# Kernel tuning notes

Hardware: AMD Instinct MI355X
Metric: run time of the kernel (lower is better)

The kernel has to match this reference:

```python
import jax, jax.numpy as jnp
import numpy as np
from jax import lax

T, B, D, H, K, A = 256, 512, 128, 50, 5, 4


def setup_inputs() -> dict:
    key = jax.random.key(0)
    ks = jax.random.split(key, 12)
    s = 0.05
    return {
        "x": jax.random.normal(ks[0], (T, B, D), dtype=jnp.float32),
        "W_in": jax.random.normal(ks[1], (H, D), dtype=jnp.float32) * s,
        "b_in": jax.random.normal(ks[2], (H,), dtype=jnp.float32) * s,
        "W_ctx": jax.random.normal(ks[3], (H, 2 * H), dtype=jnp.float32) * s,
        "b_ctx": jax.random.normal(ks[4], (H,), dtype=jnp.float32) * s,
        "W_key": jax.random.normal(ks[5], (K, H), dtype=jnp.float32) * s,
        "b_key": jax.random.normal(ks[6], (K,), dtype=jnp.float32) * s,
        "W_q": jax.random.normal(ks[7], (K, H), dtype=jnp.float32) * s,
        "b_q": jax.random.normal(ks[8], (K,), dtype=jnp.float32) * s,
        "first_context": jax.random.normal(ks[9], (H,), dtype=jnp.float32) * s,
        "W_act": jax.random.normal(ks[10], (A, H), dtype=jnp.float32) * s,
        "b_act": jax.random.normal(ks[11], (A,), dtype=jnp.float32) * s,
    }


def reference(x, W_in, b_in, W_ctx, b_ctx, W_key, b_key, W_q, b_q,
              first_context, W_act, b_act):
    # Unrolls the torch module's per-step forward() over T steps with a
    # growing attention context (horizon=-1 => attend to full history).
    Tn, Bn, _ = x.shape
    Hn = W_in.shape[0]
    Kn = W_key.shape[0]
    neg_inf = jnp.float32(-1e30)

    c0 = jnp.broadcast_to(first_context[None, :], (Bn, Hn))  # [B,H]
    ctx_buf = jnp.zeros((Tn + 1, Bn, Hn), x.dtype).at[0].set(c0)
    key_buf = jnp.zeros((Tn + 1, Bn, Kn), x.dtype).at[0].set(c0 @ W_key.T + b_key)
    step_ids = jnp.arange(Tn + 1)[:, None]  # [T+1,1]

    def step(carry, xt):
        ctx_buf, key_buf, prev_c, t = carry
        h = jax.nn.relu(xt @ W_in.T + b_in)                           # [B,H]
        c = jax.nn.relu(jnp.concatenate([prev_c, h], axis=1) @ W_ctx.T + b_ctx)
        ctx_buf = ctx_buf.at[t + 1].set(c)
        key_buf = key_buf.at[t + 1].set(c @ W_key.T + b_key)
        q = c @ W_q.T + b_q                                           # [B,K]
        scores = jnp.einsum('tbk,bk->tb', key_buf, q)                 # [T+1,B]
        scores = jnp.where(step_ids <= t + 1, scores, neg_inf)
        attn = jax.nn.softmax(scores, axis=0)                         # over history
        w = jnp.einsum('tb,tbh->bh', attn, ctx_buf)                   # [B,H]
        actions = w @ W_act.T + b_act                                 # [B,A]
        return (ctx_buf, key_buf, c, t + 1), actions

    _, actions = lax.scan(step, (ctx_buf, key_buf, c0, jnp.int32(0)), x)
    return actions  # [T,B,A]
```

## Files before the change

kernel.cpp:

```cpp
#include <hip/hip_runtime.h>

#define TT 256
#define BB 512
#define DD 128
#define HH 50
#define KK 5
#define AA 4
#define NROW 131072
#define KQS 260

#define R50(X) X(0) X(1) X(2) X(3) X(4) X(5) X(6) X(7) X(8) X(9) \
  X(10) X(11) X(12) X(13) X(14) X(15) X(16) X(17) X(18) X(19) \
  X(20) X(21) X(22) X(23) X(24) X(25) X(26) X(27) X(28) X(29) \
  X(30) X(31) X(32) X(33) X(34) X(35) X(36) X(37) X(38) X(39) \
  X(40) X(41) X(42) X(43) X(44) X(45) X(46) X(47) X(48) X(49)

typedef _Float16 half4 __attribute__((ext_vector_type(4)));
typedef float f32x4 __attribute__((ext_vector_type(4)));

__global__ void k0_prep(const float* __restrict__ W_in,
                        const float* __restrict__ W_ctx,
                        const float* __restrict__ W_key,
                        const float* __restrict__ W_q,
                        const float* __restrict__ b_key,
                        const float* __restrict__ b_q,
                        float* __restrict__ WHT,
                        float* __restrict__ WK2T, float* __restrict__ bias2) {
  int i = blockIdx.x * 256 + threadIdx.x;
  if (i < HH * 52) {
    int j = i / 52, h = i % 52;
    WHT[i] = (h < HH) ? W_ctx[h * (2 * HH) + HH + j] : 0.f;
  }
  if (i < HH * 64) {
    int j = i >> 6, l = i & 63;
    float v = 0.f;
    if (l < HH) v = W_ctx[l * (2 * HH) + j];
    else if (l < HH + KK) v = W_key[(l - HH) * HH + j];
    else if (l < HH + 2 * KK) v = W_q[(l - HH - KK) * HH + j];
    WK2T[i] = v;
  }
  if (i < 64) {
    float bv = 0.f;
    if (i >= HH && i < HH + KK) bv = b_key[i - HH];
    else if (i >= HH + KK && i < HH + 2 * KK) bv = b_q[i - HH - KK];
    bias2[i] = bv;
  }
}

__global__ __launch_bounds__(256, 2) void k1_mfma(
    const float* __restrict__ x, const float* __restrict__ W_in,
    const float* __restrict__ WHT, const float* __restrict__ b_in,
    const float* __restrict__ b_ctx, _Float16* __restrict__ gh) {
  const int lane = threadIdx.x & 63;
  const int wave = threadIdx.x >> 6;
  const int lrow = lane & 15, lgrp = lane >> 4;

#define WA1D(m, kk)                                                     \
  half4 wa1_##m##_##kk;                                                 \
  {                                                                     \
    const int hh = 16 * (m) + lrow;                                     \
    const int j0 = 16 * (kk) + 4 * lgrp;                                \
    const bool v = (hh < HH);                                           \
    const float* p = W_in + (size_t)(v ? hh : 0) * DD + j0;             \
    wa1_##m##_##kk[0] = (_Float16)(v ? p[0] : 0.f);                     \
    wa1_##m##_##kk[1] = (_Float16)(v ? p[1] : 0.f);                     \
    wa1_##m##_##kk[2] = (_Float16)(v ? p[2] : 0.f);                     \
    wa1_##m##_##kk[3] = (_Float16)(v ? p[3] : 0.f);                     \
  }
  WA1D(0, 0) WA1D(0, 1) WA1D(0, 2) WA1D(0, 3)
  WA1D(0, 4) WA1D(0, 5) WA1D(0, 6) WA1D(0, 7)
  WA1D(1, 0) WA1D(1, 1) WA1D(1, 2) WA1D(1, 3)
  WA1D(1, 4) WA1D(1, 5) WA1D(1, 6) WA1D(1, 7)
  WA1D(2, 0) WA1D(2, 1) WA1D(2, 2) WA1D(2, 3)
  WA1D(2, 4) WA1D(2, 5) WA1D(2, 6) WA1D(2, 7)
  WA1D(3, 0) WA1D(3, 1) WA1D(3, 2) WA1D(3, 3)
  WA1D(3, 4) WA1D(3, 5) WA1D(3, 6) WA1D(3, 7)

#define WA2D(m, kk)                                                     \
  half4 wa2_##m##_##kk;                                                 \
  {                                                                     \
    const int gg = 16 * (m) + lrow;                                     \
    const int h0 = 16 * (kk) + 4 * lgrp;                                \
    wa2_##m##_##kk[0] = (_Float16)((gg < HH && h0 + 0 < HH) ? WHT[(h0 + 0) * 52 + gg] : 0.f); \
    wa2_##m##_##kk[1] = (_Float16)((gg < HH && h0 + 1 < HH) ? WHT[(h0 + 1) * 52 + gg] : 0.f); \
    wa2_##m##_##kk[2] = (_Float16)((gg < HH && h0 + 2 < HH) ? WHT[(h0 + 2) * 52 + gg] : 0.f); \
    wa2_##m##_##kk[3] = (_Float16)((gg < HH && h0 + 3 < HH) ? WHT[(h0 + 3) * 52 + gg] : 0.f); \
  }
  WA2D(0, 0) WA2D(0, 1) WA2D(0, 2) WA2D(0, 3)
  WA2D(1, 0) WA2D(1, 1) WA2D(1, 2) WA2D(1, 3)
  WA2D(2, 0) WA2D(2, 1) WA2D(2, 2) WA2D(2, 3)
  WA2D(3, 0) WA2D(3, 1) WA2D(3, 2) WA2D(3, 3)

#define BDEF(m, r)                                                      \
  const float bin_##m##_##r =                                           \
      (16 * (m) + 4 * lgrp + (r) < HH) ? b_in[16 * (m) + 4 * lgrp + (r)] : 0.f; \
  const float bct_##m##_##r =                                           \
      (16 * (m) + 4 * lgrp + (r) < HH) ? b_ctx[16 * (m) + 4 * lgrp + (r)] : 0.f;
  BDEF(0, 0) BDEF(0, 1) BDEF(0, 2) BDEF(0, 3)
  BDEF(1, 0) BDEF(1, 1) BDEF(1, 2) BDEF(1, 3)
  BDEF(2, 0) BDEF(2, 1) BDEF(2, 2) BDEF(2, 3)
  BDEF(3, 0) BDEF(3, 1) BDEF(3, 2) BDEF(3, 3)

  const f32x4 zf = {0.f, 0.f, 0.f, 0.f};

#pragma unroll 1
  for (int it = 0; it < 4; ++it) {
    const int tile = (blockIdx.x * 4 + wave) * 4 + it;
    const int row = tile * 16 + lrow;
    const float* __restrict__ xr = x + (size_t)row * DD + 4 * lgrp;

#define XLD(kk)                                                         \
  half4 xb##kk;                                                         \
  {                                                                     \
    const float4 xv = *reinterpret_cast<const float4*>(xr + 16 * kk);   \
    xb##kk[0] = (_Float16)xv.x;                                         \
    xb##kk[1] = (_Float16)xv.y;                                         \
    xb##kk[2] = (_Float16)xv.z;                                         \
    xb##kk[3] = (_Float16)xv.w;                                         \
  }
    XLD(0) XLD(1) XLD(2) XLD(3) XLD(4) XLD(5) XLD(6) XLD(7)

    f32x4 d10 = zf, d11 = zf, d12 = zf, d13 = zf;
#define MM1(kk)                                                              \
  d10 = __builtin_amdgcn_mfma_f32_16x16x16f16(wa1_0_##kk, xb##kk, d10, 0, 0, 0); \
  d11 = __builtin_amdgcn_mfma_f32_16x16x16f16(wa1_1_##kk, xb##kk, d11, 0, 0, 0); \
  d12 = __builtin_amdgcn_mfma_f32_16x16x16f16(wa1_2_##kk, xb##kk, d12, 0, 0, 0); \
  d13 = __builtin_amdgcn_mfma_f32_16x16x16f16(wa1_3_##kk, xb##kk, d13, 0, 0, 0);
    MM1(0) MM1(1) MM1(2) MM1(3) MM1(4) MM1(5) MM1(6) MM1(7)

#define HBD(k)                                                    \
  half4 hb##k;                                                    \
  hb##k[0] = (_Float16)fmaxf(d1##k[0] + bin_##k##_0, 0.f);        \
  hb##k[1] = (_Float16)fmaxf(d1##k[1] + bin_##k##_1, 0.f);        \
  hb##k[2] = (_Float16)fmaxf(d1##k[2] + bin_##k##_2, 0.f);        \
  hb##k[3] = (_Float16)fmaxf(d1##k[3] + bin_##k##_3, 0.f);
    HBD(0) HBD(1) HBD(2) HBD(3)

    f32x4 d20 = zf, d21 = zf, d22 = zf, d23 = zf;
#define MM2(kk)                                                              \
  d20 = __builtin_amdgcn_mfma_f32_16x16x16f16(wa2_0_##kk, hb##kk, d20, 0, 0, 0); \
  d21 = __builtin_amdgcn_mfma_f32_16x16x16f16(wa2_1_##kk, hb##kk, d21, 0, 0, 0); \
  d22 = __builtin_amdgcn_mfma_f32_16x16x16f16(wa2_2_##kk, hb##kk, d22, 0, 0, 0); \
  d23 = __builtin_amdgcn_mfma_f32_16x16x16f16(wa2_3_##kk, hb##kk, d23, 0, 0, 0);
    MM2(0) MM2(1) MM2(2) MM2(3)

    _Float16* __restrict__ gr =
        gh + ((size_t)(row & (BB - 1)) * TT + (row >> 9)) * 64;
#define GST4(off, D, B0, B1, B2, B3)                          \
  {                                                           \
    half4 v;                                                  \
    v[0] = (_Float16)(D[0] + B0);                             \
    v[1] = (_Float16)(D[1] + B1);                             \
    v[2] = (_Float16)(D[2] + B2);                             \
    v[3] = (_Float16)(D[3] + B3);                             \
    *reinterpret_cast<half4*>(gr + (off) + 4 * lgrp) = v;     \
  }
    GST4(0, d20, bct_0_0, bct_0_1, bct_0_2, bct_0_3)
    GST4(16, d21, bct_1_0, bct_1_1, bct_1_2, bct_1_3)
    GST4(32, d22, bct_2_0, bct_2_1, bct_2_2, bct_2_3)
    {
      half4 v;
      v[0] = (_Float16)((lgrp == 0) ? d23[0] + bct_3_0 : 0.f);
      v[1] = (_Float16)((lgrp == 0) ? d23[1] + bct_3_1 : 0.f);
      v[2] = (_Float16)0.f;
      v[3] = (_Float16)0.f;
      *reinterpret_cast<half4*>(gr + 48 + 4 * lgrp) = v;
    }
  }
}

__global__ __launch_bounds__(64) void k2_rec(
    const _Float16* __restrict__ gh, const float* __restrict__ WK2T,
    const float* __restrict__ bias2, const float* __restrict__ first_context,
    float* __restrict__ ctxg64, float* __restrict__ kqg) {
  __shared__ __align__(16) float c_lds[64];
  const int b = blockIdx.x;
  const int lane = threadIdx.x;

#define WDECL(j)                            \
  float w##j = WK2T[(j) * 64 + lane];       \
  asm volatile("" : "+v"(w##j));
  R50(WDECL)
  const float wz = 0.f;
  const float bias = bias2[lane];

  const float c0v = (lane < HH) ? first_context[lane] : 0.f;
  c_lds[lane] = c0v;
  ctxg64[((size_t)b * 257 + 0) * 64 + lane] = c0v;

  const _Float16* __restrict__ gbp = gh + (size_t)b * TT * 64 + lane;
  float gq0 = (float)gbp[0 * 64];
  float gq1 = (float)gbp[1 * 64];
  float gq2 = (float)gbp[2 * 64];
  float gq3 = (float)gbp[3 * 64];
  float gq4 = (float)gbp[4 * 64];
  float gq5 = (float)gbp[5 * 64];
  float gq6 = (float)gbp[6 * 64];
  float gq7 = (float)gbp[7 * 64];

  float* __restrict__ ctp = ctxg64 + (size_t)b * 257 * 64 + lane;
  const bool iskq = (lane >= HH && lane < HH + 2 * KK);
  float* __restrict__ kqrow =
      kqg + ((size_t)b * 10 + (iskq ? lane - HH : 0)) * KQS;

#define KQ(J, wa, wb, wc, wd)                                            \
  {                                                                      \
    const float4 cq = *reinterpret_cast<const float4*>(&c_lds[J]);       \
    acc0 = fmaf(wa, cq.x, acc0);                                         \
    acc1 = fmaf(wb, cq.y, acc1);                                         \
    acc2 = fmaf(wc, cq.z, acc2);                                         \
    acc3 = fmaf(wd, cq.w, acc3);                                         \
  }
#define DOT50R                                                           \
  float acc0 = 0.f, acc1 = 0.f, acc2 = 0.f, acc3 = 0.f;                  \
  KQ(0, w0, w1, w2, w3) KQ(4, w4, w5, w6, w7)                            \
  KQ(8, w8, w9, w10, w11) KQ(12, w12, w13, w14, w15)                     \
  KQ(16, w16, w17, w18, w19) KQ(20, w20, w21, w22, w23)                  \
  KQ(24, w24, w25, w26, w27) KQ(28, w28, w29, w30, w31)                  \
  KQ(32, w32, w33, w34, w35) KQ(36, w36, w37, w38, w39)                  \
  KQ(40, w40, w41, w42, w43) KQ(44, w44, w45, w46, w47)                  \
  KQ(48, w48, w49, wz, wz)                                               \
  const float acc = (acc0 + acc1) + (acc2 + acc3);

#define BODY(RR, GQ)                                                     \
  {                                                                      \
    const int t = tg8 + RR;                                              \
    DOT50R                                                               \
    kqa##RR = acc + bias;                                                \
    const float cn = fmaxf(acc + GQ, 0.f);                               \
    GQ = (float)gbp[(size_t)min(t + 8, TT - 1) * 64];                    \
    ctp[(size_t)(t + 1) * 64] = cn;                                      \
    c_lds[lane] = cn;           \
  }

#pragma unroll 1
  for (int tg8 = 0; tg8 < TT; tg8 += 8) {
    float kqa0, kqa1, kqa2, kqa3, kqa4, kqa5, kqa6, kqa7;
    BODY(0, gq0) BODY(1, gq1) BODY(2, gq2) BODY(3, gq3)
    BODY(4, gq4) BODY(5, gq5) BODY(6, gq6) BODY(7, gq7)
    if (iskq) {
      *reinterpret_cast<float4*>(kqrow + tg8) =
          make_float4(kqa0, kqa1, kqa2, kqa3);
      *reinterpret_cast<float4*>(kqrow + tg8 + 4) =
          make_float4(kqa4, kqa5, kqa6, kqa7);
    }
  }

  {
    DOT50R
    if (iskq) kqrow[TT] = acc + bias;
  }
}

__global__ __launch_bounds__(256, 4) void k3_attn(
    const float* __restrict__ ctxg64, const float* __restrict__ kqg,
    const float* __restrict__ W_act, const float* __restrict__ b_act,
    float* __restrict__ out) {
  __shared__ __align__(16) float ct[64 * 66];
  __shared__ __align__(16) float k_l[16 * 68];
  __shared__ __align__(16) float o_l[64 * 66];
  __shared__ float su_l[64];

  const int tid = threadIdx.x;
  const int bid = blockIdx.x;
  const int chunk = 3 - (bid >> 9);
  const int b = bid & 511;
  const int tbase = chunk * 64;
  const int nst = min(tbase + 66, 257);
  const int ntiles = (nst + 63) >> 6;
  const int wave = tid >> 6;
  const int lane = tid & 63;
  const int lrow = lane & 15;
  const int lgrp = lane >> 4;
  const int tw = tbase + wave * 16;

  for (int i = tid; i < 11 * 68; i += 256) k_l[5 * 68 + i] = 0.f;

  half4 qf;
#pragma unroll
  for (int i = 0; i < 4; ++i) {
    const int k = 4 * lgrp + i;
    qf[i] = (_Float16)((k < KK)
                           ? kqg[((size_t)b * 10 + 5 + k) * KQS + tw + lrow + 1]
                           : 0.f);
  }

  const f32x4 zf = {0.f, 0.f, 0.f, 0.f};
  f32x4 acc0 = zf, acc1 = zf, acc2 = zf, acc3 = zf;
  float su = 0.f;

#pragma unroll 1
  for (int tile = 0; tile < ntiles; ++tile) {
    __syncthreads();
    {
      const int r = tid >> 2;
      const int c0 = (tid & 3) * 16;
      const int srow = tile * 64 + r;
      const float* src = ctxg64 + ((size_t)b * 257 + srow) * 64;
      const bool sv = (srow < nst);
#pragma unroll
      for (int u = 0; u < 8; ++u) {
        const int c = c0 + u * 2;
        float2 v = make_float2(0.f, 0.f);
        if (sv && c < HH) v = *reinterpret_cast<const float2*>(src + c);
        *reinterpret_cast<float2*>(&ct[r * 66 + c]) = v;
      }
    }
    {
      for (int i = tid; i < KK * 64; i += 256) {
        const int k = i >> 6, sl = i & 63;
        const int s = tile * 64 + sl;
        k_l[k * 68 + sl] =
            (s <= TT) ? kqg[((size_t)b * 10 + k) * KQS + s] : 0.f;
      }
    }
    __syncthreads();

    if (tile * 64 <= tw + 16) {
#pragma unroll 1
      for (int su16 = 0; su16 < 4; ++su16) {
        const int sb = tile * 64 + su16 * 16;
        if (sb > tw + 16) break;

        half4 kf;
#pragma unroll
        for (int i = 0; i < 4; ++i)
          kf[i] = (_Float16)k_l[(4 * lgrp + i) * 68 + su16 * 16 + lrow];

        const f32x4 sc =
            __builtin_amdgcn_mfma_f32_16x16x16f16(kf, qf, zf, 0, 0, 0);

        half4 pa;
#pragma unroll
        for (int r = 0; r < 4; ++r) {
          const int s = sb + 4 * lgrp + r;
          const float p = (s <= tw + lrow + 1) ? __expf(sc[r]) : 0.f;
          su += p;
          pa[r] = (_Float16)p;
        }

        const int vbase = su16 * 16 + 4 * lgrp;
#define PVHT(HT, ACC)                                                     \
  {                                                                       \
    half4 vf;                                                             \
    vf[0] = (_Float16)ct[(vbase + 0) * 66 + lrow + 16 * HT];              \
    vf[1] = (_Float16)ct[(vbase + 1) * 66 + lrow + 16 * HT];              \
    vf[2] = (_Float16)ct[(vbase + 2) * 66 + lrow + 16 * HT];              \
    vf[3] = (_Float16)ct[(vbase + 3) * 66 + lrow + 16 * HT];              \
    ACC = __builtin_amdgcn_mfma_f32_16x16x16f16(pa, vf, ACC, 0, 0, 0);    \
  }
        PVHT(0, acc0) PVHT(1, acc1) PVHT(2, acc2) PVHT(3, acc3)
      }
    }
  }

  su += __shfl_xor(su, 16, 64);
  su += __shfl_xor(su, 32, 64);
  if (lane < 16) su_l[wave * 16 + lane] = su;

#pragma unroll
  for (int r = 0; r < 4; ++r) {
    const int trow = wave * 16 + 4 * lgrp + r;
    o_l[trow * 66 + lrow + 0] = acc0[r];
    o_l[trow * 66 + lrow + 16] = acc1[r];
    o_l[trow * 66 + lrow + 32] = acc2[r];
    o_l[trow * 66 + lrow + 48] = acc3[r];
  }
  __syncthreads();

  {
    const int tl = tid >> 2;
    const int a = tid & 3;
    const float inv = 1.f / su_l[tl];
    const float* orow = &o_l[tl * 66];
    const float* wrow = W_act + a * HH;
    float s0 = 0.f, s1 = 0.f;
#pragma unroll
    for (int h = 0; h < HH; h += 2) {
      s0 = fmaf(orow[h], wrow[h], s0);
      s1 = fmaf(orow[h + 1], wrow[h + 1], s1);
    }
    out[((size_t)(tbase + tl) * BB + b) * AA + a] =
        fmaf(s0 + s1, inv, b_act[a]);
  }
}

extern "C" void kernel_launch(void* const* d_in, const int* in_sizes, int n_in,
                              void* d_out, int out_size, void* d_ws,
                              size_t ws_size, hipStream_t stream) {
  const float* x = (const float*)d_in[0];
  const float* W_in = (const float*)d_in[1];
  const float* b_in = (const float*)d_in[2];
  const float* W_ctx = (const float*)d_in[3];
  const float* b_ctx = (const float*)d_in[4];
  const float* W_key = (const float*)d_in[5];
  const float* b_key = (const float*)d_in[6];
  const float* W_q = (const float*)d_in[7];
  const float* b_q = (const float*)d_in[8];
  const float* fc = (const float*)d_in[9];
  const float* W_act = (const float*)d_in[10];
  const float* b_act = (const float*)d_in[11];
  float* out = (float*)d_out;
  float* ws = (float*)d_ws;

  float* WHT = ws;
  float* WK2T = ws + 4096;
  float* bias2 = ws + 8128;
  _Float16* gh = (_Float16*)(ws + 8192);
  float* ctxg64 = ws + 8192 + 4194304;
  float* kqg = ctxg64 + (size_t)BB * 257 * 64;

  hipLaunchKernelGGL(k0_prep, dim3(26), dim3(256), 0, stream, W_in, W_ctx,
                     W_key, W_q, b_key, b_q, WHT, WK2T, bias2);
  hipLaunchKernelGGL(k1_mfma, dim3(512), dim3(256), 0, stream, x, W_in, WHT,
                     b_in, b_ctx, gh);
  hipLaunchKernelGGL(k2_rec, dim3(512), dim3(64), 0, stream, gh, WK2T, bias2,
                     fc, ctxg64, kqg);
  hipLaunchKernelGGL(k3_attn, dim3(2048), dim3(256), 0, stream, ctxg64, kqg,
                     W_act, b_act, out);
}
```

Before: 161.2 us.

## Batch recurrence across 16 chains with fp16 MFMA and time-major buffers

Replaces the per-batch scalar recurrence kernel (one 64-lane wave per batch element, 512 blocks) with an MFMA version where each wave advances 16 batch chains at once using 16x16x16 fp16 matrix ops. The context and key/query buffers become time-major, and the attention kernel's indexing is updated to match. This cuts the serial FMA and LDS round-trip cost per step but launches only 32 waves, so most CUs sit idle during the recurrence. It also rounds the recurrent state to fp16 on every step, which adds precision risk.

```diff
diff --git a/kernel.cpp b/kernel.cpp
--- a/kernel.cpp
+++ b/kernel.cpp
@@ -7,13 +7,6 @@
 #define KK 5
 #define AA 4
 #define NROW 131072
-#define KQS 260
-
-#define R50(X) X(0) X(1) X(2) X(3) X(4) X(5) X(6) X(7) X(8) X(9) \
-  X(10) X(11) X(12) X(13) X(14) X(15) X(16) X(17) X(18) X(19) \
-  X(20) X(21) X(22) X(23) X(24) X(25) X(26) X(27) X(28) X(29) \
-  X(30) X(31) X(32) X(33) X(34) X(35) X(36) X(37) X(38) X(39) \
-  X(40) X(41) X(42) X(43) X(44) X(45) X(46) X(47) X(48) X(49)
 
 typedef _Float16 half4 __attribute__((ext_vector_type(4)));
 typedef float f32x4 __attribute__((ext_vector_type(4)));
@@ -169,91 +162,145 @@
   }
 }
 
-__global__ __launch_bounds__(64) void k2_rec(
+__global__ __launch_bounds__(64, 1) void k2_mfma(
     const _Float16* __restrict__ gh, const float* __restrict__ WK2T,
-    const float* __restrict__ bias2, const float* __restrict__ first_context,
-    float* __restrict__ ctxg64, float* __restrict__ kqg) {
-  __shared__ __align__(16) float c_lds[64];
-  const int b = blockIdx.x;
+    const float* __restrict__ bias2, const float* __restrict__ fc,
+    float* __restrict__ ctxT, float* __restrict__ kqT) {
   const int lane = threadIdx.x;
-
-#define WDECL(j)                            \
-  float w##j = WK2T[(j) * 64 + lane];       \
-  asm volatile("" : "+v"(w##j));
-  R50(WDECL)
-  const float wz = 0.f;
-  const float bias = bias2[lane];
-
-  const float c0v = (lane < HH) ? first_context[lane] : 0.f;
-  c_lds[lane] = c0v;
-  ctxg64[((size_t)b * 257 + 0) * 64 + lane] = c0v;
-
-  const _Float16* __restrict__ gbp = gh + (size_t)b * TT * 64 + lane;
-  float gq0 = (float)gbp[0 * 64];
-  float gq1 = (float)gbp[1 * 64];
-  float gq2 = (float)gbp[2 * 64];
-  float gq3 = (float)gbp[3 * 64];
-  float gq4 = (float)gbp[4 * 64];
-  float gq5 = (float)gbp[5 * 64];
-  float gq6 = (float)gbp[6 * 64];
-  float gq7 = (float)gbp[7 * 64];
-
-  float* __restrict__ ctp = ctxg64 + (size_t)b * 257 * 64 + lane;
-  const bool iskq = (lane >= HH && lane < HH + 2 * KK);
-  float* __restrict__ kqrow =
-      kqg + ((size_t)b * 10 + (iskq ? lane - HH : 0)) * KQS;
-
-#define KQ(J, wa, wb, wc, wd)                                            \
-  {                                                                      \
-    const float4 cq = *reinterpret_cast<const float4*>(&c_lds[J]);       \
-    acc0 = fmaf(wa, cq.x, acc0);                                         \
-    acc1 = fmaf(wb, cq.y, acc1);                                         \
-    acc2 = fmaf(wc, cq.z, acc2);                                         \
-    acc3 = fmaf(wd, cq.w, acc3);                                         \
-  }
-#define DOT50R                                                           \
-  float acc0 = 0.f, acc1 = 0.f, acc2 = 0.f, acc3 = 0.f;                  \
-  KQ(0, w0, w1, w2, w3) KQ(4, w4, w5, w6, w7)                            \
-  KQ(8, w8, w9, w10, w11) KQ(12, w12, w13, w14, w15)                     \
-  KQ(16, w16, w17, w18, w19) KQ(20, w20, w21, w22, w23)                  \
-  KQ(24, w24, w25, w26, w27) KQ(28, w28, w29, w30, w31)                  \
-  KQ(32, w32, w33, w34, w35) KQ(36, w36, w37, w38, w39)                  \
-  KQ(40, w40, w41, w42, w43) KQ(44, w44, w45, w46, w47)                  \
-  KQ(48, w48, w49, wz, wz)                                               \
-  const float acc = (acc0 + acc1) + (acc2 + acc3);
-
-#define BODY(RR, GQ)                                                     \
-  {                                                                      \
-    const int t = tg8 + RR;                                              \
-    DOT50R                                                               \
-    kqa##RR = acc + bias;                                                \
-    const float cn = fmaxf(acc + GQ, 0.f);                               \
-    GQ = (float)gbp[(size_t)min(t + 8, TT - 1) * 64];                    \
-    ctp[(size_t)(t + 1) * 64] = cn;                                      \
-    c_lds[lane] = cn;           \
+  const int lrow = lane & 15, lgrp = lane >> 4;
+  const int chain0 = blockIdx.x * 16;
+  const int chain = chain0 + lrow;
+
+#define DECLWF(m, kk)                                                       \
+  half4 wf_##m##_##kk;                                                      \
+  {                                                                         \
+    const int j0 = (kk) * 16 + 4 * lgrp;                                    \
+    wf_##m##_##kk[0] = (_Float16)((j0 + 0 < HH) ? WK2T[(j0 + 0) * 64 + (m) * 16 + lrow] : 0.f); \
+    wf_##m##_##kk[1] = (_Float16)((j0 + 1 < HH) ? WK2T[(j0 + 1) * 64 + (m) * 16 + lrow] : 0.f); \
+    wf_##m##_##kk[2] = (_Float16)((j0 + 2 < HH) ? WK2T[(j0 + 2) * 64 + (m) * 16 + lrow] : 0.f); \
+    wf_##m##_##kk[3] = (_Float16)((j0 + 3 < HH) ? WK2T[(j0 + 3) * 64 + (m) * 16 + lrow] : 0.f); \
+  }
+  DECLWF(0, 0) DECLWF(0, 1) DECLWF(0, 2) DECLWF(0, 3)
+  DECLWF(1, 0) DECLWF(1, 1) DECLWF(1, 2) DECLWF(1, 3)
+  DECLWF(2, 0) DECLWF(2, 1) DECLWF(2, 2) DECLWF(2, 3)
+  DECLWF(3, 0) DECLWF(3, 1) DECLWF(3, 2) DECLWF(3, 3)
+
+  const float bias_0 = bias2[48 + 4 * lgrp + 0];
+  const float bias_1 = bias2[48 + 4 * lgrp + 1];
+  const float bias_2 = bias2[48 + 4 * lgrp + 2];
+  const float bias_3 = bias2[48 + 4 * lgrp + 3];
+#define KQR(r)                                            \
+  const int row_##r = 48 + 4 * lgrp + r;                  \
+  const bool kv_##r = (row_##r >= 50 && row_##r < 60);
+  KQR(0) KQR(1) KQR(2) KQR(3)
+
+#define DECLBF(kk)                                                  \
+  half4 bf_##kk;                                                    \
+  {                                                                 \
+    const int j0 = (kk) * 16 + 4 * lgrp;                            \
+    bf_##kk[0] = (_Float16)((j0 + 0 < HH) ? fc[j0 + 0] : 0.f);      \
+    bf_##kk[1] = (_Float16)((j0 + 1 < HH) ? fc[j0 + 1] : 0.f);      \
+    bf_##kk[2] = (_Float16)((j0 + 2 < HH) ? fc[j0 + 2] : 0.f);      \
+    bf_##kk[3] = (_Float16)((j0 + 3 < HH) ? fc[j0 + 3] : 0.f);      \
+  }
+  DECLBF(0) DECLBF(1) DECLBF(2) DECLBF(3)
+
+  for (int i = lane; i < 16 * 64; i += 64) {
+    const int c = i >> 6, h = i & 63;
+    ctxT[((size_t)0 * BB + chain0 + c) * 64 + h] = (h < HH) ? fc[h] : 0.f;
+  }
+
+  const _Float16* __restrict__ ghp = gh + (size_t)chain * TT * 64 + 4 * lgrp;
+
+  half4 gA0 = *(const half4*)(ghp + 0 * 64 + 0);
+  half4 gA1 = *(const half4*)(ghp + 0 * 64 + 16);
+  half4 gA2 = *(const half4*)(ghp + 0 * 64 + 32);
+  half4 gA3 = *(const half4*)(ghp + 0 * 64 + 48);
+  half4 gB0 = *(const half4*)(ghp + 1 * 64 + 0);
+  half4 gB1 = *(const half4*)(ghp + 1 * 64 + 16);
+  half4 gB2 = *(const half4*)(ghp + 1 * 64 + 32);
+  half4 gB3 = *(const half4*)(ghp + 1 * 64 + 48);
+
+  const f32x4 zf = {0.f, 0.f, 0.f, 0.f};
+
+#define MM(D, A, B) D = __builtin_amdgcn_mfma_f32_16x16x16f16(A, B, D, 0, 0, 0);
+#define MSTEP(T, G0, G1, G2, G3, TPF)                                      \
+  {                                                                        \
+    f32x4 d0 = zf, d1 = zf, d2 = zf, d3 = zf;                              \
+    MM(d0, wf_0_0, bf_0) MM(d1, wf_1_0, bf_0)                              \
+    MM(d2, wf_2_0, bf_0) MM(d3, wf_3_0, bf_0)                              \
+    MM(d0, wf_0_1, bf_1) MM(d1, wf_1_1, bf_1)                              \
+    MM(d2, wf_2_1, bf_1) MM(d3, wf_3_1, bf_1)                              \
+    MM(d0, wf_0_2, bf_2) MM(d1, wf_1_2, bf_2)                              \
+    MM(d2, wf_2_2, bf_2) MM(d3, wf_3_2, bf_2)                              \
+    MM(d0, wf_0_3, bf_3) MM(d1, wf_1_3, bf_3)                              \
+    MM(d2, wf_2_3, bf_3) MM(d3, wf_3_3, bf_3)                              \
+    {                                                                      \
+      float* kqo = kqT + ((size_t)(T) * BB + chain) * 12;                  \
+      if (kv_0) kqo[row_0 - 50] = d3[0] + bias_0;                          \
+      if (kv_1) kqo[row_1 - 50] = d3[1] + bias_1;                          \
+      if (kv_2) kqo[row_2 - 50] = d3[2] + bias_2;                          \
+      if (kv_3) kqo[row_3 - 50] = d3[3] + bias_3;                          \
+    }                                                                      \
+    const float cn_0_0 = fmaxf(d0[0] + (float)G0[0], 0.f);                 \
+    const float cn_0_1 = fmaxf(d0[1] + (float)G0[1], 0.f);                 \
+    const float cn_0_2 = fmaxf(d0[2] + (float)G0[2], 0.f);                 \
+    const float cn_0_3 = fmaxf(d0[3] + (float)G0[3], 0.f);                 \
+    const float cn_1_0 = fmaxf(d1[0] + (float)G1[0], 0.f);                 \
+    const float cn_1_1 = fmaxf(d1[1] + (float)G1[1], 0.f);                 \
+    const float cn_1_2 = fmaxf(d1[2] + (float)G1[2], 0.f);                 \
+    const float cn_1_3 = fmaxf(d1[3] + (float)G1[3], 0.f);                 \
+    const float cn_2_0 = fmaxf(d2[0] + (float)G2[0], 0.f);                 \
+    const float cn_2_1 = fmaxf(d2[1] + (float)G2[1], 0.f);                 \
+    const float cn_2_2 = fmaxf(d2[2] + (float)G2[2], 0.f);                 \
+    const float cn_2_3 = fmaxf(d2[3] + (float)G2[3], 0.f);                 \
+    const float cn_3_0 = fmaxf(d3[0] + (float)G3[0], 0.f);                 \
+    const float cn_3_1 = fmaxf(d3[1] + (float)G3[1], 0.f);                 \
+    const float cn_3_2 = fmaxf(d3[2] + (float)G3[2], 0.f);                 \
+    const float cn_3_3 = fmaxf(d3[3] + (float)G3[3], 0.f);                 \
+    G0 = *(const half4*)(ghp + (size_t)((TPF) < TT ? (TPF) : TT - 1) * 64 + 0);  \
+    G1 = *(const half4*)(ghp + (size_t)((TPF) < TT ? (TPF) : TT - 1) * 64 + 16); \
+    G2 = *(const half4*)(ghp + (size_t)((TPF) < TT ? (TPF) : TT - 1) * 64 + 32); \
+    G3 = *(const half4*)(ghp + (size_t)((TPF) < TT ? (TPF) : TT - 1) * 64 + 48); \
+    float* cto = ctxT + ((size_t)((T) + 1) * BB + chain) * 64 + 4 * lgrp;  \
+    *reinterpret_cast<float4*>(cto + 0) =                                  \
+        make_float4(cn_0_0, cn_0_1, cn_0_2, cn_0_3);                       \
+    *reinterpret_cast<float4*>(cto + 16) =                                 \
+        make_float4(cn_1_0, cn_1_1, cn_1_2, cn_1_3);                       \
+    *reinterpret_cast<float4*>(cto + 32) =                                 \
+        make_float4(cn_2_0, cn_2_1, cn_2_2, cn_2_3);                       \
+    *reinterpret_cast<float4*>(cto + 48) =                                 \
+        make_float4(cn_3_0, cn_3_1, cn_3_2, cn_3_3);                       \
+    bf_0[0] = (_Float16)cn_0_0; bf_0[1] = (_Float16)cn_0_1;                \
+    bf_0[2] = (_Float16)cn_0_2; bf_0[3] = (_Float16)cn_0_3;                \
+    bf_1[0] = (_Float16)cn_1_0; bf_1[1] = (_Float16)cn_1_1;                \
+    bf_1[2] = (_Float16)cn_1_2; bf_1[3] = (_Float16)cn_1_3;                \
+    bf_2[0] = (_Float16)cn_2_0; bf_2[1] = (_Float16)cn_2_1;                \
+    bf_2[2] = (_Float16)cn_2_2; bf_2[3] = (_Float16)cn_2_3;                \
+    bf_3[0] = (_Float16)cn_3_0; bf_3[1] = (_Float16)cn_3_1;                \
+    bf_3[2] = (_Float16)cn_3_2; bf_3[3] = (_Float16)cn_3_3;                \
   }
 
 #pragma unroll 1
-  for (int tg8 = 0; tg8 < TT; tg8 += 8) {
-    float kqa0, kqa1, kqa2, kqa3, kqa4, kqa5, kqa6, kqa7;
-    BODY(0, gq0) BODY(1, gq1) BODY(2, gq2) BODY(3, gq3)
-    BODY(4, gq4) BODY(5, gq5) BODY(6, gq6) BODY(7, gq7)
-    if (iskq) {
-      *reinterpret_cast<float4*>(kqrow + tg8) =
-          make_float4(kqa0, kqa1, kqa2, kqa3);
-      *reinterpret_cast<float4*>(kqrow + tg8 + 4) =
-          make_float4(kqa4, kqa5, kqa6, kqa7);
-    }
+  for (int t = 0; t < TT; t += 2) {
+    MSTEP(t, gA0, gA1, gA2, gA3, t + 2)
+    MSTEP(t + 1, gB0, gB1, gB2, gB3, t + 3)
   }
 
   {
-    DOT50R
-    if (iskq) kqrow[TT] = acc + bias;
+    f32x4 d3 = zf;
+    MM(d3, wf_3_0, bf_0) MM(d3, wf_3_1, bf_1)
+    MM(d3, wf_3_2, bf_2) MM(d3, wf_3_3, bf_3)
+    float* kqo = kqT + ((size_t)TT * BB + chain) * 12;
+    if (kv_0) kqo[row_0 - 50] = d3[0] + bias_0;
+    if (kv_1) kqo[row_1 - 50] = d3[1] + bias_1;
+    if (kv_2) kqo[row_2 - 50] = d3[2] + bias_2;
+    if (kv_3) kqo[row_3 - 50] = d3[3] + bias_3;
   }
 }
 
 __global__ __launch_bounds__(256, 4) void k3_attn(
-    const float* __restrict__ ctxg64, const float* __restrict__ kqg,
+    const float* __restrict__ ctxT, const float* __restrict__ kqT,
     const float* __restrict__ W_act, const float* __restrict__ b_act,
     float* __restrict__ out) {
   __shared__ __align__(16) float ct[64 * 66];
@@ -280,9 +327,8 @@
 #pragma unroll
   for (int i = 0; i < 4; ++i) {
     const int k = 4 * lgrp + i;
-    qf[i] = (_Float16)((k < KK)
-                           ? kqg[((size_t)b * 10 + 5 + k) * KQS + tw + lrow + 1]
-                           : 0.f);
+    qf[i] = (_Float16)(
+        (k < KK) ? kqT[((size_t)(tw + lrow + 1) * BB + b) * 12 + 5 + k] : 0.f);
   }
 
   const f32x4 zf = {0.f, 0.f, 0.f, 0.f};
@@ -296,7 +342,7 @@
       const int r = tid >> 2;
       const int c0 = (tid & 3) * 16;
       const int srow = tile * 64 + r;
-      const float* src = ctxg64 + ((size_t)b * 257 + srow) * 64;
+      const float* src = ctxT + ((size_t)srow * BB + b) * 64;
       const bool sv = (srow < nst);
 #pragma unroll
       for (int u = 0; u < 8; ++u) {
@@ -311,7 +357,7 @@
         const int k = i >> 6, sl = i & 63;
         const int s = tile * 64 + sl;
         k_l[k * 68 + sl] =
-            (s <= TT) ? kqg[((size_t)b * 10 + k) * KQS + s] : 0.f;
+            (s <= TT) ? kqT[((size_t)s * BB + b) * 12 + k] : 0.f;
       }
     }
     __syncthreads();
@@ -407,15 +453,15 @@
   float* WK2T = ws + 4096;
   float* bias2 = ws + 8128;
   _Float16* gh = (_Float16*)(ws + 8192);
-  float* ctxg64 = ws + 8192 + 4194304;
-  float* kqg = ctxg64 + (size_t)BB * 257 * 64;
+  float* ctxT = ws + 8192 + 4194304;
+  float* kqT = ctxT + (size_t)257 * BB * 64;
 
   hipLaunchKernelGGL(k0_prep, dim3(26), dim3(256), 0, stream, W_in, W_ctx,
                      W_key, W_q, b_key, b_q, WHT, WK2T, bias2);
   hipLaunchKernelGGL(k1_mfma, dim3(512), dim3(256), 0, stream, x, W_in, WHT,
                      b_in, b_ctx, gh);
-  hipLaunchKernelGGL(k2_rec, dim3(512), dim3(64), 0, stream, gh, WK2T, bias2,
-                     fc, ctxg64, kqg);
-  hipLaunchKernelGGL(k3_attn, dim3(2048), dim3(256), 0, stream, ctxg64, kqg,
+  hipLaunchKernelGGL(k2_mfma, dim3(32), dim3(64), 0, stream, gh, WK2T, bias2,
+                     fc, ctxT, kqT);
+  hipLaunchKernelGGL(k3_attn, dim3(2048), dim3(256), 0, stream, ctxT, kqT,
                      W_act, b_act, out);
 }
```

Measured after the change: 209.2 us. 29.8% more time.
